# Performance work log

Measured on AMD Instinct MI355X. Metric: run time of the kernel, lower is better.

The kernel has to match this reference:

```python
import jax, jax.numpy as jnp
import numpy as np

N_NODES = 100000
N_EDGES = 1600000
IN_F, HID, EMB = 128, 64, 32


def setup_inputs() -> dict:
    key = jax.random.key(0)
    ks = jax.random.split(key, 10)
    x = jax.random.normal(ks[0], (N_NODES, IN_F), dtype=jnp.float32)
    edge_index = jax.random.randint(ks[1], (2, N_EDGES), 0, N_NODES, dtype=jnp.int64)
    s = lambda k, sh, fan_in: jax.random.normal(k, sh, dtype=jnp.float32) / jnp.sqrt(jnp.float32(fan_in))
    return {
        "x": x,
        "edge_index": edge_index,
        # SAGEConv1: lin_l (applied to aggregated neighbors, with bias) + lin_r (root, no bias)
        "W1_l": s(ks[2], (IN_F, HID), IN_F), "b1": jnp.zeros((HID,), jnp.float32), "W1_r": s(ks[3], (IN_F, HID), IN_F),
        # SAGEConv2
        "W2_l": s(ks[4], (HID, EMB), HID), "b2": jnp.zeros((EMB,), jnp.float32), "W2_r": s(ks[5], (HID, EMB), HID),
        # risk head
        "Wh": s(ks[6], (EMB, 1), EMB), "bh": jnp.zeros((1,), jnp.float32),
    }


def _sage_conv(x, src, dst, W_l, b, W_r):
    # gather messages from source nodes, segment-mean at destination nodes
    msg_sum = jax.ops.segment_sum(x[src], dst, num_segments=N_NODES)  # [N, F]
    cnt = jax.ops.segment_sum(jnp.ones((src.shape[0],), x.dtype), dst, num_segments=N_NODES)
    mean_agg = msg_sum / jnp.maximum(cnt, 1.0)[:, None]  # isolated nodes -> 0
    return mean_agg @ W_l + b + x @ W_r


def reference(x, edge_index, W1_l, b1, W1_r, W2_l, b2, W2_r, Wh, bh):
    src, dst = edge_index[0], edge_index[1]
    h = jax.nn.relu(_sage_conv(x, src, dst, W1_l, b1, W1_r))
    # dropout is identity in eval mode
    embeddings = jax.nn.relu(_sage_conv(h, src, dst, W2_l, b2, W2_r))
    risk_scores = embeddings @ Wh + bh
    return embeddings, risk_scores
```

## Files before the change

### kernel.cpp

```cpp
#include <hip/hip_runtime.h>
#include <hip/hip_bf16.h>

#define N_NODES 100000
#define N_EDGES 1600000
#define NBUCK   391
#define BSHIFT  8
#define BCAP    6144

typedef __bf16 bf16x8 __attribute__((ext_vector_type(8)));
typedef float  f32x4  __attribute__((ext_vector_type(4)));
typedef float  f32x2  __attribute__((ext_vector_type(2)));


__device__ inline unsigned char enc_fp8(float v) {
    return (unsigned char)(__builtin_amdgcn_cvt_pk_fp8_f32(v, v, 0, 0) & 0xFF);
}

__global__ __launch_bounds__(256) void partition_k(const int* __restrict__ ei,
                                                   int* __restrict__ gcur,
                                                   unsigned* __restrict__ bbuf) {
    __shared__ int hist[NBUCK];
    __shared__ int cur[NBUCK];
    int t = threadIdx.x;
    for (int i = t; i < NBUCK; i += 256) hist[i] = 0;
    __syncthreads();
    int base = blockIdx.x * 4096;
    unsigned pk[16];
    int bk[16];
#pragma unroll
    for (int i = 0; i < 16; ++i) {
        int e = base + t + i * 256;
        if (e < N_EDGES) {
            int s = ei[e], d = ei[N_EDGES + e];
            int b = d >> BSHIFT;
            pk[i] = ((unsigned)(d & 255) << 17) | (unsigned)s;
            bk[i] = b;
            atomicAdd(&hist[b], 1);
        } else bk[i] = -1;
    }
    __syncthreads();
    for (int i = t; i < NBUCK; i += 256)
        cur[i] = atomicAdd(&gcur[i], hist[i]);
    __syncthreads();
#pragma unroll
    for (int i = 0; i < 16; ++i) {
        if (bk[i] >= 0) {
            int pos = atomicAdd(&cur[bk[i]], 1);
            bbuf[(size_t)bk[i] * BCAP + pos] = pk[i];
        }
    }
}

__global__ __launch_bounds__(256) void csr_gemm1_k(const unsigned* __restrict__ bbuf,
                                                   const int* __restrict__ gcur,
                                                   int* __restrict__ cnt,
                                                   int* __restrict__ offsets,
                                                   int* __restrict__ csr,
                                                   const float* __restrict__ x,
                                                   const float* __restrict__ W1l,
                                                   const float* __restrict__ W1r,
                                                   unsigned char* __restrict__ c1l,
                                                   __bf16* __restrict__ c1r) {
    __shared__ __align__(16) char smem[34816];
    int t = threadIdx.x;
    if (blockIdx.x < NBUCK) {
        int* lcnt = (int*)smem;
        int* lcur = (int*)(smem + 1024);
        int* ssum = (int*)(smem + 2048);
        int b = blockIdx.x;
        int m = gcur[b];
        const unsigned* src = bbuf + (size_t)b * BCAP;
        lcnt[t] = 0;
        __syncthreads();
        for (int i = t; i < m; i += 256) atomicAdd(&lcnt[src[i] >> 17], 1);
        __syncthreads();
        int a0 = lcnt[t];
        ssum[t] = (a0 + 3) & ~3;
        __syncthreads();
        for (int off = 1; off < 256; off <<= 1) {
            int v = (t >= off) ? ssum[t - off] : 0;
            __syncthreads();
            ssum[t] += v;
            __syncthreads();
        }
        int ebase = (t == 0) ? 0 : ssum[t - 1];
        lcur[t] = ebase;
        int n = (b << BSHIFT) + t;
        if (n < N_NODES) {
            cnt[n] = a0;
            offsets[n] = b * BCAP + ebase;
        }
        __syncthreads();
        for (int i = t; i < m; i += 256) {
            unsigned p = src[i];
            int pos = atomicAdd(&lcur[p >> 17], 1);
            csr[(size_t)b * BCAP + pos] = (int)(p & 0x1FFFF);
        }
    } else {
        __bf16* Bt = (__bf16*)smem;
        for (int idx = t; idx < 8192; idx += 256) {
            int k = idx >> 6, n = idx & 63;
            Bt[n * 136 + k]        = (__bf16)W1l[idx];
            Bt[(n + 64) * 136 + k] = (__bf16)W1r[idx];
        }
        __syncthreads();

        int lane = t & 63, wave = t >> 6;
        int bid = blockIdx.x - NBUCK;
        int mbase = bid * 64 + wave * 16;
        int col  = lane & 15;
        int kgrp = (lane >> 4) << 3;
        int mrow = mbase + col;
        int mclamp = mrow < N_NODES ? mrow : N_NODES - 1;
        const float* arow = x + (size_t)mclamp * 128;

        f32x4 acc[8];
#pragma unroll
        for (int i = 0; i < 8; ++i) acc[i] = (f32x4){0.f, 0.f, 0.f, 0.f};

#pragma unroll
        for (int ks = 0; ks < 4; ++ks) {
            int kk = ks * 32 + kgrp;
            f32x4 a0 = *(const f32x4*)(arow + kk);
            f32x4 a1 = *(const f32x4*)(arow + kk + 4);
            bf16x8 a;
#pragma unroll
            for (int i = 0; i < 4; ++i) { a[i] = (__bf16)a0[i]; a[i + 4] = (__bf16)a1[i]; }
#pragma unroll
            for (int nt = 0; nt < 8; ++nt) {
                bf16x8 b = *(const bf16x8*)(Bt + (nt * 16 + col) * 136 + kk);
                acc[nt] = __builtin_amdgcn_mfma_f32_16x16x32_bf16(a, b, acc[nt], 0, 0, 0);
            }
        }

        int r0 = mbase + ((lane >> 4) << 2);
#pragma unroll
        for (int r = 0; r < 4; ++r) {
            int m = r0 + r;
            if (m < N_NODES) {
#pragma unroll
                for (int nt = 0; nt < 4; ++nt)
                    c1l[(size_t)m * 64 + nt * 16 + col] = enc_fp8(acc[nt][r]);
#pragma unroll
                for (int nt = 4; nt < 8; ++nt)
                    c1r[(size_t)m * 64 + (nt - 4) * 16 + col] = (__bf16)acc[nt][r];
            }
        }
    }
}

__global__ __launch_bounds__(256) void agg1_gemm2_k(const unsigned char* __restrict__ c1l,
                                                    const __bf16* __restrict__ c1r,
                                                    const int* __restrict__ offsets,
                                                    const int* __restrict__ cnt,
                                                    const int* __restrict__ csr,
                                                    const float* __restrict__ b1,
                                                    const float* __restrict__ W2l,
                                                    const float* __restrict__ W2r,
                                                    unsigned char* __restrict__ c2l,
                                                    float* __restrict__ c2r) {
    __shared__ __bf16 Bt[64 * 72];
    __shared__ __bf16 ht[64 * 76];
    int tid = threadIdx.x;
    for (int idx = tid; idx < 2048; idx += 256) {
        int k = idx >> 5, n = idx & 31;
        Bt[n * 72 + k]        = (__bf16)W2l[idx];
        Bt[(n + 32) * 72 + k] = (__bf16)W2r[idx];
    }

    int lane = tid & 63, wave = tid >> 6;
    int g = lane >> 3;
    int f8b = (lane & 7) << 3;
    f32x4 b1v0 = *(const f32x4*)(b1 + f8b);
    f32x4 b1v1 = *(const f32x4*)(b1 + f8b + 4);
    const int4* csr4 = (const int4*)csr;
#pragma unroll
    for (int p = 0; p < 2; ++p) {
        int lrow = p * 32 + wave * 8 + g;
        int n = blockIdx.x * 64 + lrow;
        bf16x8 o;
        if (n < N_NODES) {
            int beg = offsets[n], deg = cnt[n];
            int end = beg + deg;
            bf16x8 rv = *(const bf16x8*)(c1r + (size_t)n * 64 + f8b);
            int4 j0 = csr4[beg >> 2];
            int4 j1 = csr4[(beg >> 2) + 1];
            float sum[8];
#pragma unroll
            for (int j = 0; j < 8; ++j) sum[j] = 0.f;
            for (int e = beg; e < end; e += 8) {
                int4 i0 = j0, i1 = j1;
                j0 = csr4[(e >> 2) + 2];
                j1 = csr4[(e >> 2) + 3];
                int sidx[8] = {i0.x, i0.y, i0.z, i0.w, i1.x, i1.y, i1.z, i1.w};
                uint2 w[8];
#pragma unroll
                for (int u = 0; u < 8; ++u) {
                    w[u].x = 0u; w[u].y = 0u;
                    if (e + u < end)
                        w[u] = *(const uint2*)(c1l + (size_t)sidx[u] * 64 + f8b);
                }
#pragma unroll
                for (int u = 0; u < 8; ++u) {
                    f32x2 p0 = __builtin_amdgcn_cvt_pk_f32_fp8(w[u].x, 0);
                    f32x2 p1 = __builtin_amdgcn_cvt_pk_f32_fp8(w[u].x, 1);
                    f32x2 p2 = __builtin_amdgcn_cvt_pk_f32_fp8(w[u].y, 0);
                    f32x2 p3 = __builtin_amdgcn_cvt_pk_f32_fp8(w[u].y, 1);
                    sum[0] += p0[0]; sum[1] += p0[1];
                    sum[2] += p1[0]; sum[3] += p1[1];
                    sum[4] += p2[0]; sum[5] += p2[1];
                    sum[6] += p3[0]; sum[7] += p3[1];
                }
            }
            float cf = deg > 0 ? (float)deg : 1.f;
#pragma unroll
            for (int j = 0; j < 8; ++j) {
                float v = sum[j] / cf + (float)rv[j] + ((j < 4) ? b1v0[j] : b1v1[j - 4]);
                o[j] = (__bf16)(v > 0.f ? v : 0.f);
            }
        } else {
#pragma unroll
            for (int j = 0; j < 8; ++j) o[j] = (__bf16)0.f;
        }
        *(bf16x8*)(ht + lrow * 76 + f8b) = o;
    }
    __syncthreads();

    int col  = lane & 15;
    int kgrp = (lane >> 4) << 3;
    int mbase = blockIdx.x * 64 + wave * 16;
    const __bf16* arow = ht + (wave * 16 + col) * 76;

    f32x4 acc[4];
#pragma unroll
    for (int i = 0; i < 4; ++i) acc[i] = (f32x4){0.f, 0.f, 0.f, 0.f};

#pragma unroll
    for (int ks = 0; ks < 2; ++ks) {
        int kk = ks * 32 + kgrp;
        bf16x8 a = *(const bf16x8*)(arow + kk);
#pragma unroll
        for (int nt = 0; nt < 4; ++nt) {
            bf16x8 b = *(const bf16x8*)(Bt + (nt * 16 + col) * 72 + kk);
            acc[nt] = __builtin_amdgcn_mfma_f32_16x16x32_bf16(a, b, acc[nt], 0, 0, 0);
        }
    }

    int r0 = mbase + ((lane >> 4) << 2);
#pragma unroll
    for (int r = 0; r < 4; ++r) {
        int m = r0 + r;
        if (m < N_NODES) {
#pragma unroll
            for (int nt = 0; nt < 2; ++nt)
                c2l[(size_t)m * 32 + nt * 16 + col] = enc_fp8(acc[nt][r]);
#pragma unroll
            for (int nt = 2; nt < 4; ++nt)
                c2r[(size_t)m * 32 + (nt - 2) * 16 + col] = acc[nt][r];
        }
    }
}

__global__ __launch_bounds__(256) void agg2_k(const unsigned char* __restrict__ c2l,
                                              const float* __restrict__ c2r,
                                              const int* __restrict__ offsets,
                                              const int* __restrict__ cnt,
                                              const int* __restrict__ csr,
                                              const float* __restrict__ b2,
                                              const float* __restrict__ Wh,
                                              const float* __restrict__ bh,
                                              float* __restrict__ out) {
    int wave = blockIdx.x * 4 + (threadIdx.x >> 6);
    int lane = threadIdx.x & 63;
    int g = lane >> 2;
    int n = wave * 16 + g;
    int f8b = (lane & 3) << 3;
    bool valid = n < N_NODES;
    int nc = valid ? n : N_NODES - 1;
    int beg = offsets[nc], deg = valid ? cnt[n] : 0;
    int end = beg + deg;
    f32x4 rr0 = *(const f32x4*)(c2r + (size_t)nc * 32 + f8b);
    f32x4 rr1 = *(const f32x4*)(c2r + (size_t)nc * 32 + f8b + 4);
    f32x4 wh0 = *(const f32x4*)(Wh + f8b);
    f32x4 wh1 = *(const f32x4*)(Wh + f8b + 4);
    const int4* csr4 = (const int4*)csr;
    int4 j0 = csr4[beg >> 2];
    int4 j1 = csr4[(beg >> 2) + 1];
    float sum[8];
#pragma unroll
    for (int j = 0; j < 8; ++j) sum[j] = 0.f;
    for (int e = beg; e < end; e += 8) {
        int4 i0 = j0, i1 = j1;
        j0 = csr4[(e >> 2) + 2];
        j1 = csr4[(e >> 2) + 3];
        int sidx[8] = {i0.x, i0.y, i0.z, i0.w, i1.x, i1.y, i1.z, i1.w};
        uint2 w[8];
#pragma unroll
        for (int u = 0; u < 8; ++u) {
            w[u].x = 0u; w[u].y = 0u;
            if (e + u < end)
                w[u] = *(const uint2*)(c2l + (size_t)sidx[u] * 32 + f8b);
        }
#pragma unroll
        for (int u = 0; u < 8; ++u) {
            f32x2 p0 = __builtin_amdgcn_cvt_pk_f32_fp8(w[u].x, 0);
            f32x2 p1 = __builtin_amdgcn_cvt_pk_f32_fp8(w[u].x, 1);
            f32x2 p2 = __builtin_amdgcn_cvt_pk_f32_fp8(w[u].y, 0);
            f32x2 p3 = __builtin_amdgcn_cvt_pk_f32_fp8(w[u].y, 1);
            sum[0] += p0[0]; sum[1] += p0[1];
            sum[2] += p1[0]; sum[3] += p1[1];
            sum[4] += p2[0]; sum[5] += p2[1];
            sum[6] += p3[0]; sum[7] += p3[1];
        }
    }
    float cf = deg > 0 ? (float)deg : 1.f;
    float r = 0.f;
    f32x4 o0, o1;
#pragma unroll
    for (int j = 0; j < 8; ++j) {
        float root = (j < 4) ? rr0[j] : rr1[j - 4];
        float whj  = (j < 4) ? wh0[j] : wh1[j - 4];
        float v = sum[j] / cf + root + b2[f8b + j];
        v = v > 0.f ? v : 0.f;
        if (j < 4) o0[j] = v; else o1[j - 4] = v;
        r += v * whj;
    }
    if (valid) {
        *(f32x4*)(out + (size_t)n * 32 + f8b) = o0;
        *(f32x4*)(out + (size_t)n * 32 + f8b + 4) = o1;
    }
    r += __shfl_xor(r, 1, 64);
    r += __shfl_xor(r, 2, 64);
    if (valid && (lane & 3) == 0)
        out[(size_t)N_NODES * 32 + n] = r + bh[0];
}

extern "C" void kernel_launch(void* const* d_in, const int* in_sizes, int n_in,
                              void* d_out, int out_size, void* d_ws, size_t ws_size,
                              hipStream_t stream) {
    const float* x   = (const float*)d_in[0];
    const int*   ei  = (const int*)d_in[1];
    const float* W1l = (const float*)d_in[2];
    const float* b1  = (const float*)d_in[3];
    const float* W1r = (const float*)d_in[4];
    const float* W2l = (const float*)d_in[5];
    const float* b2  = (const float*)d_in[6];
    const float* W2r = (const float*)d_in[7];
    const float* Wh  = (const float*)d_in[8];
    const float* bh  = (const float*)d_in[9];
    float* out = (float*)d_out;

    char* ws = (char*)d_ws;
    unsigned char* c1l = (unsigned char*)(ws);
    __bf16*   c1r     = (__bf16*)(ws + 6400000);
    unsigned char* c2l = (unsigned char*)(ws + 32000000);
    float*    c2r     = (float*)(ws + 35200000);
    int*      cnt     = (int*)(ws + 48000000);
    int*      offsets = (int*)(ws + 48400000);
    int*      gcur    = (int*)(ws + 48800000);
    unsigned* bbuf    = (unsigned*)(ws + 48804096);
    int*      csr     = (int*)(ws + 58437888);

    hipMemsetAsync(gcur, 0, NBUCK * 4, stream);

    partition_k  <<<391, 256, 0, stream>>>(ei, gcur, bbuf);
    csr_gemm1_k  <<<NBUCK + 1563, 256, 0, stream>>>(bbuf, gcur, cnt, offsets, csr,
                                                    x, W1l, W1r, c1l, c1r);
    agg1_gemm2_k <<<1563, 256, 0, stream>>>(c1l, c1r, offsets, cnt, csr, b1,
                                            W2l, W2r, c2l, c2r);
    agg2_k       <<<1563, 256, 0, stream>>>(c2l, c2r, offsets, cnt, csr, b2, Wh, bh, out);
}
```

Before: 204.5 us.

## Split GEMM1 across partition and CSR kernels, halve bucket size to 128 nodes

Half of the first-layer GEMM tiles now run as extra blocks in the partition kernel, the other half in the CSR-build kernel, so both kernels mix memory-bound edge work with MFMA work. Bucket granularity drops from 256 to 128 destination nodes (782 buckets, capacity 3072), which doubles the number of CSR blocks and halves per-bucket work. The risks are more global atomics on bucket counters, larger per-block histograms in the partition phase, and per-bucket capacity overflow if a bucket exceeds 3072 edges.

```diff
diff --git a/kernel.cpp b/kernel.cpp
--- a/kernel.cpp
+++ b/kernel.cpp
@@ -3,9 +3,9 @@
 
 #define N_NODES 100000
 #define N_EDGES 1600000
-#define NBUCK   391
-#define BSHIFT  8
-#define BCAP    6144
+#define NBUCK   782
+#define BSHIFT  7
+#define BCAP    3072
 
 typedef __bf16 bf16x8 __attribute__((ext_vector_type(8)));
 typedef float  f32x4  __attribute__((ext_vector_type(4)));
@@ -16,79 +16,148 @@
     return (unsigned char)(__builtin_amdgcn_cvt_pk_fp8_f32(v, v, 0, 0) & 0xFF);
 }
 
-__global__ __launch_bounds__(256) void partition_k(const int* __restrict__ ei,
-                                                   int* __restrict__ gcur,
-                                                   unsigned* __restrict__ bbuf) {
-    __shared__ int hist[NBUCK];
-    __shared__ int cur[NBUCK];
+__device__ inline void gemm1_tile(const __bf16* Bt, const float* __restrict__ x,
+                                  unsigned char* __restrict__ c1l,
+                                  __bf16* __restrict__ c1r,
+                                  int mbase, int lane, int wave) {
+    int col  = lane & 15;
+    int kgrp = (lane >> 4) << 3;
+    int mrow = mbase + wave * 16 + col;
+    int mclamp = mrow < N_NODES ? mrow : N_NODES - 1;
+    const float* arow = x + (size_t)mclamp * 128;
+
+    f32x4 acc[8];
+#pragma unroll
+    for (int i = 0; i < 8; ++i) acc[i] = (f32x4){0.f, 0.f, 0.f, 0.f};
+
+#pragma unroll
+    for (int ks = 0; ks < 4; ++ks) {
+        int kk = ks * 32 + kgrp;
+        f32x4 a0 = *(const f32x4*)(arow + kk);
+        f32x4 a1 = *(const f32x4*)(arow + kk + 4);
+        bf16x8 a;
+#pragma unroll
+        for (int i = 0; i < 4; ++i) { a[i] = (__bf16)a0[i]; a[i + 4] = (__bf16)a1[i]; }
+#pragma unroll
+        for (int nt = 0; nt < 8; ++nt) {
+            bf16x8 b = *(const bf16x8*)(Bt + (nt * 16 + col) * 136 + kk);
+            acc[nt] = __builtin_amdgcn_mfma_f32_16x16x32_bf16(a, b, acc[nt], 0, 0, 0);
+        }
+    }
+
+    int r0 = mbase + wave * 16 + ((lane >> 4) << 2);
+#pragma unroll
+    for (int r = 0; r < 4; ++r) {
+        int m = r0 + r;
+        if (m < N_NODES) {
+#pragma unroll
+            for (int nt = 0; nt < 4; ++nt)
+                c1l[(size_t)m * 64 + nt * 16 + col] = enc_fp8(acc[nt][r]);
+#pragma unroll
+            for (int nt = 4; nt < 8; ++nt)
+                c1r[(size_t)m * 64 + (nt - 4) * 16 + col] = (__bf16)acc[nt][r];
+        }
+    }
+}
+
+__device__ inline void stage_W1(__bf16* Bt, const float* __restrict__ W1l,
+                                const float* __restrict__ W1r, int t) {
+    for (int idx = t; idx < 8192; idx += 256) {
+        int k = idx >> 6, n = idx & 63;
+        Bt[n * 136 + k]        = (__bf16)W1l[idx];
+        Bt[(n + 64) * 136 + k] = (__bf16)W1r[idx];
+    }
+}
+
+__global__ __launch_bounds__(256) void part_gemm1a_k(const int* __restrict__ ei,
+                                                     int* __restrict__ gcur,
+                                                     unsigned* __restrict__ bbuf,
+                                                     const float* __restrict__ x,
+                                                     const float* __restrict__ W1l,
+                                                     const float* __restrict__ W1r,
+                                                     unsigned char* __restrict__ c1l,
+                                                     __bf16* __restrict__ c1r) {
+    __shared__ __align__(16) char smem[34816];
     int t = threadIdx.x;
-    for (int i = t; i < NBUCK; i += 256) hist[i] = 0;
-    __syncthreads();
-    int base = blockIdx.x * 4096;
-    unsigned pk[16];
-    int bk[16];
-#pragma unroll
-    for (int i = 0; i < 16; ++i) {
-        int e = base + t + i * 256;
-        if (e < N_EDGES) {
-            int s = ei[e], d = ei[N_EDGES + e];
-            int b = d >> BSHIFT;
-            pk[i] = ((unsigned)(d & 255) << 17) | (unsigned)s;
-            bk[i] = b;
-            atomicAdd(&hist[b], 1);
-        } else bk[i] = -1;
-    }
-    __syncthreads();
-    for (int i = t; i < NBUCK; i += 256)
-        cur[i] = atomicAdd(&gcur[i], hist[i]);
-    __syncthreads();
-#pragma unroll
-    for (int i = 0; i < 16; ++i) {
-        if (bk[i] >= 0) {
-            int pos = atomicAdd(&cur[bk[i]], 1);
-            bbuf[(size_t)bk[i] * BCAP + pos] = pk[i];
-        }
-    }
-}
-
-__global__ __launch_bounds__(256) void csr_gemm1_k(const unsigned* __restrict__ bbuf,
-                                                   const int* __restrict__ gcur,
-                                                   int* __restrict__ cnt,
-                                                   int* __restrict__ offsets,
-                                                   int* __restrict__ csr,
-                                                   const float* __restrict__ x,
-                                                   const float* __restrict__ W1l,
-                                                   const float* __restrict__ W1r,
-                                                   unsigned char* __restrict__ c1l,
-                                                   __bf16* __restrict__ c1r) {
+    if (blockIdx.x < 391) {
+        int* hist = (int*)smem;
+        int* cur  = (int*)(smem + 3328);
+        for (int i = t; i < NBUCK; i += 256) hist[i] = 0;
+        __syncthreads();
+        int base = blockIdx.x * 4096;
+        unsigned pk[16];
+        int bk[16];
+#pragma unroll
+        for (int i = 0; i < 16; ++i) {
+            int e = base + t + i * 256;
+            if (e < N_EDGES) {
+                int s = ei[e], d = ei[N_EDGES + e];
+                int b = d >> BSHIFT;
+                pk[i] = ((unsigned)(d & 127) << 17) | (unsigned)s;
+                bk[i] = b;
+                atomicAdd(&hist[b], 1);
+            } else bk[i] = -1;
+        }
+        __syncthreads();
+        for (int i = t; i < NBUCK; i += 256)
+            cur[i] = atomicAdd(&gcur[i], hist[i]);
+        __syncthreads();
+#pragma unroll
+        for (int i = 0; i < 16; ++i) {
+            if (bk[i] >= 0) {
+                int pos = atomicAdd(&cur[bk[i]], 1);
+                bbuf[(size_t)bk[i] * BCAP + pos] = pk[i];
+            }
+        }
+    } else {
+        __bf16* Bt = (__bf16*)smem;
+        stage_W1(Bt, W1l, W1r, t);
+        __syncthreads();
+        int mbase = (blockIdx.x - 391) * 64;
+        gemm1_tile(Bt, x, c1l, c1r, mbase, t & 63, t >> 6);
+    }
+}
+
+__global__ __launch_bounds__(256) void csr_gemm1b_k(const unsigned* __restrict__ bbuf,
+                                                    const int* __restrict__ gcur,
+                                                    int* __restrict__ cnt,
+                                                    int* __restrict__ offsets,
+                                                    int* __restrict__ csr,
+                                                    const float* __restrict__ x,
+                                                    const float* __restrict__ W1l,
+                                                    const float* __restrict__ W1r,
+                                                    unsigned char* __restrict__ c1l,
+                                                    __bf16* __restrict__ c1r) {
     __shared__ __align__(16) char smem[34816];
     int t = threadIdx.x;
     if (blockIdx.x < NBUCK) {
         int* lcnt = (int*)smem;
-        int* lcur = (int*)(smem + 1024);
-        int* ssum = (int*)(smem + 2048);
+        int* lcur = (int*)(smem + 512);
+        int* ssum = (int*)(smem + 1024);
         int b = blockIdx.x;
         int m = gcur[b];
         const unsigned* src = bbuf + (size_t)b * BCAP;
-        lcnt[t] = 0;
+        if (t < 128) lcnt[t] = 0;
         __syncthreads();
         for (int i = t; i < m; i += 256) atomicAdd(&lcnt[src[i] >> 17], 1);
         __syncthreads();
-        int a0 = lcnt[t];
-        ssum[t] = (a0 + 3) & ~3;
-        __syncthreads();
-        for (int off = 1; off < 256; off <<= 1) {
-            int v = (t >= off) ? ssum[t - off] : 0;
+        int a0 = 0;
+        if (t < 128) { a0 = lcnt[t]; ssum[t] = (a0 + 3) & ~3; }
+        __syncthreads();
+        for (int off = 1; off < 128; off <<= 1) {
+            int v = (t < 128 && t >= off) ? ssum[t - off] : 0;
             __syncthreads();
-            ssum[t] += v;
+            if (t < 128) ssum[t] += v;
             __syncthreads();
         }
-        int ebase = (t == 0) ? 0 : ssum[t - 1];
-        lcur[t] = ebase;
-        int n = (b << BSHIFT) + t;
-        if (n < N_NODES) {
-            cnt[n] = a0;
-            offsets[n] = b * BCAP + ebase;
+        if (t < 128) {
+            int ebase = (t == 0) ? 0 : ssum[t - 1];
+            lcur[t] = ebase;
+            int n = (b << BSHIFT) + t;
+            if (n < N_NODES) {
+                cnt[n] = a0;
+                offsets[n] = b * BCAP + ebase;
+            }
         }
         __syncthreads();
         for (int i = t; i < m; i += 256) {
@@ -98,54 +167,10 @@
         }
     } else {
         __bf16* Bt = (__bf16*)smem;
-        for (int idx = t; idx < 8192; idx += 256) {
-            int k = idx >> 6, n = idx & 63;
-            Bt[n * 136 + k]        = (__bf16)W1l[idx];
-            Bt[(n + 64) * 136 + k] = (__bf16)W1r[idx];
-        }
-        __syncthreads();
-
-        int lane = t & 63, wave = t >> 6;
-        int bid = blockIdx.x - NBUCK;
-        int mbase = bid * 64 + wave * 16;
-        int col  = lane & 15;
-        int kgrp = (lane >> 4) << 3;
-        int mrow = mbase + col;
-        int mclamp = mrow < N_NODES ? mrow : N_NODES - 1;
-        const float* arow = x + (size_t)mclamp * 128;
-
-        f32x4 acc[8];
-#pragma unroll
-        for (int i = 0; i < 8; ++i) acc[i] = (f32x4){0.f, 0.f, 0.f, 0.f};
-
-#pragma unroll
-        for (int ks = 0; ks < 4; ++ks) {
-            int kk = ks * 32 + kgrp;
-            f32x4 a0 = *(const f32x4*)(arow + kk);
-            f32x4 a1 = *(const f32x4*)(arow + kk + 4);
-            bf16x8 a;
-#pragma unroll
-            for (int i = 0; i < 4; ++i) { a[i] = (__bf16)a0[i]; a[i + 4] = (__bf16)a1[i]; }
-#pragma unroll
-            for (int nt = 0; nt < 8; ++nt) {
-                bf16x8 b = *(const bf16x8*)(Bt + (nt * 16 + col) * 136 + kk);
-                acc[nt] = __builtin_amdgcn_mfma_f32_16x16x32_bf16(a, b, acc[nt], 0, 0, 0);
-            }
-        }
-
-        int r0 = mbase + ((lane >> 4) << 2);
-#pragma unroll
-        for (int r = 0; r < 4; ++r) {
-            int m = r0 + r;
-            if (m < N_NODES) {
-#pragma unroll
-                for (int nt = 0; nt < 4; ++nt)
-                    c1l[(size_t)m * 64 + nt * 16 + col] = enc_fp8(acc[nt][r]);
-#pragma unroll
-                for (int nt = 4; nt < 8; ++nt)
-                    c1r[(size_t)m * 64 + (nt - 4) * 16 + col] = (__bf16)acc[nt][r];
-            }
-        }
+        stage_W1(Bt, W1l, W1r, t);
+        __syncthreads();
+        int mbase = 50048 + (blockIdx.x - NBUCK) * 64;
+        gemm1_tile(Bt, x, c1l, c1r, mbase, t & 63, t >> 6);
     }
 }
 
@@ -363,9 +388,10 @@
 
     hipMemsetAsync(gcur, 0, NBUCK * 4, stream);
 
-    partition_k  <<<391, 256, 0, stream>>>(ei, gcur, bbuf);
-    csr_gemm1_k  <<<NBUCK + 1563, 256, 0, stream>>>(bbuf, gcur, cnt, offsets, csr,
-                                                    x, W1l, W1r, c1l, c1r);
+    part_gemm1a_k<<<391 + 782, 256, 0, stream>>>(ei, gcur, bbuf,
+                                                 x, W1l, W1r, c1l, c1r);
+    csr_gemm1b_k <<<NBUCK + 781, 256, 0, stream>>>(bbuf, gcur, cnt, offsets, csr,
+                                                   x, W1l, W1r, c1l, c1r);
     agg1_gemm2_k <<<1563, 256, 0, stream>>>(c1l, c1r, offsets, cnt, csr, b1,
                                             W2l, W2r, c2l, c2r);
     agg2_k       <<<1563, 256, 0, stream>>>(c2l, c2r, offsets, cnt, csr, b2, Wh, bh, out);
```

After: 204.1 us. About the same (-0.2%).
